# Performance work log

Measured on AMD Instinct MI355X. Metric: run time of the kernel, lower is better.

## Reference

```python
import jax, jax.numpy as jnp
import numpy as np

MAX_PAIRS = 130816  # = L*(L-1)//2 for L=512; matches init max_pairs


def setup_inputs() -> dict:
    key = jax.random.key(0)
    k1, k2, k3, k4, k5 = jax.random.split(key, 5)
    B, L, H = 32, 512, 1024
    hidden_states = jax.random.normal(k1, (B, L, H), dtype=jnp.float32)
    attention_mask = jax.random.randint(k2, (B, L), 0, 2, dtype=jnp.int32)
    special_tokens_mask = jax.random.randint(k3, (B, L), 0, 2, dtype=jnp.int32)
    # nn.Bilinear(H, H, 1): weight (1, H, H) -> squeeze to (H, H); bias (1,)
    bound = 1.0 / np.sqrt(H)
    W = jax.random.uniform(k4, (H, H), dtype=jnp.float32, minval=-bound, maxval=bound)
    b = jax.random.uniform(k5, (1,), dtype=jnp.float32, minval=-bound, maxval=bound)
    return {"hidden_states": hidden_states, "attention_mask": attention_mask,
            "special_tokens_mask": special_tokens_mask, "W": W, "b": b}


def reference(hidden_states, attention_mask, special_tokens_mask, W, b):
    # Dropout is identity in eval mode (reference assumes inference math).
    B, L, H = hidden_states.shape
    m = (attention_mask == 1) & (special_tokens_mask == 0)  # (B, L) valid AA positions

    # Bilinear score for every (t, s) pair: S[b,t,s] = h_t^T W h_s + bias
    u = jnp.einsum('blh,hk->blk', hidden_states, W)          # (B, L, H)
    S = jnp.einsum('blk,bmk->blm', u, hidden_states) + b[0]  # (B, L, L)

    # Compacted rank of each valid position (order-preserving, like nonzero()).
    r = jnp.cumsum(m.astype(jnp.int32), axis=-1) - 1          # (B, L)
    n = jnp.sum(m.astype(jnp.int32), axis=-1)[:, None, None]  # (B, 1, 1) = n_aa

    pos = jnp.arange(L, dtype=jnp.int32)
    # pair valid iff both positions are AA and t < s (compacted order preserves original order)
    valid = m[:, :, None] & m[:, None, :] & (pos[:, None] < pos[None, :])  # (B, L, L)

    i = r[:, :, None]  # compacted row index (B, L, 1)
    j = r[:, None, :]  # compacted col index (B, 1, L)
    # row-major upper-triangle (offset=1) linear index, matching torch.triu_indices order
    idx = i * (n - 1) - (i * (i - 1)) // 2 + (j - i - 1)
    idx = jnp.where(valid, idx, MAX_PAIRS)  # invalid pairs -> dump slot

    def scatter_one(s_row, ix_row):
        out = jnp.zeros((MAX_PAIRS + 1,), dtype=s_row.dtype)
        out = out.at[ix_row.reshape(-1)].set(s_row.reshape(-1))
        return out[:MAX_PAIRS]

    return jax.vmap(scatter_one)(S, idx)  # (B, MAX_PAIRS)
```

## Files before the change

kernel.cpp:

```cpp
#include <hip/hip_runtime.h>
#include <hip/hip_bf16.h>

constexpr int NB   = 32;
constexpr int LL   = 512;
constexpr int HH   = 1024;
constexpr int MAXP = 130816;
constexpr int RMAX = 256;

typedef __attribute__((ext_vector_type(8))) short short8;
typedef __attribute__((ext_vector_type(4))) float f32x4;

static __device__ inline unsigned short f2bf(float f) {
    __hip_bfloat16 h = __float2bfloat16(f);
    union { __hip_bfloat16 h; unsigned short u; } cv; cv.h = h;
    return cv.u;
}

#define GLOAD16(g, l) __builtin_amdgcn_global_load_lds( \
    (const __attribute__((address_space(1))) unsigned int*)(g), \
    (__attribute__((address_space(3))) unsigned int*)(l), 16, 0, 0)

constexpr int NGB = NB * (RMAX / 2);

__global__ __launch_bounds__(512) void prep_gather_kernel(
        const float* __restrict__ hs, const int* __restrict__ am,
        const int* __restrict__ sm, const float* __restrict__ W,
        unsigned short* __restrict__ wt, int* __restrict__ ncnt,
        unsigned short* __restrict__ hc) {
    int bi = blockIdx.x;
    if (bi < NGB) {
        int b = bi >> 7;
        int i0 = (bi & 127) * 2;
        int t = threadIdx.x;
        bool m = (am[b * LL + t] == 1) && (sm[b * LL + t] == 0);
        unsigned long long bal = __ballot(m);
        int lane = t & 63;
        int w = t >> 6;
        __shared__ int wtot[8];
        __shared__ int shg[2];
        if (lane == 0) wtot[w] = __popcll(bal);
        __syncthreads();
        int off = 0, n = 0;
        #pragma unroll
        for (int q = 0; q < 8; ++q) {
            int v = wtot[q];
            if (q < w) off += v;
            n += v;
        }
        n = min(n, RMAX);
        int npad = min(RMAX, (n + 63) & ~63);
        if (i0 == 0 && t == 0) ncnt[b] = n;
        if (i0 >= npad) return;
        int r = off + __popcll(bal & ((1ULL << lane) - 1ULL));
        if (m) {
            if (r == i0)     shg[0] = t;
            else if (r == i0 + 1) shg[1] = t;
        }
        __syncthreads();
        int half = t >> 8;
        int i = i0 + half;
        int tc = t & 255;
        ushort4 o; o.x = 0; o.y = 0; o.z = 0; o.w = 0;
        if (i < n) {
            int g = shg[half];
            float4 v = *(const float4*)(hs + ((size_t)b * LL + g) * HH + tc * 4);
            o.x = f2bf(v.x); o.y = f2bf(v.y); o.z = f2bf(v.z); o.w = f2bf(v.w);
        }
        *(ushort4*)(hc + ((size_t)b * RMAX + i) * HH + tc * 4) = o;
    } else {
        __shared__ float T[64][65];
        int tile = bi - NGB;
        int th = tile >> 4, tj = tile & 15;
        int t = threadIdx.x;
        int r = t >> 3;
        int c8 = (t & 7) * 8;
        float4 v0 = *(const float4*)(W + (size_t)(th * 64 + r) * HH + tj * 64 + c8);
        float4 v1 = *(const float4*)(W + (size_t)(th * 64 + r) * HH + tj * 64 + c8 + 4);
        T[r][c8 + 0] = v0.x; T[r][c8 + 1] = v0.y; T[r][c8 + 2] = v0.z; T[r][c8 + 3] = v0.w;
        T[r][c8 + 4] = v1.x; T[r][c8 + 5] = v1.y; T[r][c8 + 6] = v1.z; T[r][c8 + 7] = v1.w;
        __syncthreads();
        ushort4 o0, o1;
        o0.x = f2bf(T[c8 + 0][r]); o0.y = f2bf(T[c8 + 1][r]);
        o0.z = f2bf(T[c8 + 2][r]); o0.w = f2bf(T[c8 + 3][r]);
        o1.x = f2bf(T[c8 + 4][r]); o1.y = f2bf(T[c8 + 5][r]);
        o1.z = f2bf(T[c8 + 6][r]); o1.w = f2bf(T[c8 + 7][r]);
        unsigned short* dst = wt + (size_t)(tj * 64 + r) * HH + th * 64 + c8;
        *(ushort4*)dst = o0;
        *(ushort4*)(dst + 4) = o1;
    }
}

__global__ __launch_bounds__(256) void gemm1_kernel(
        const unsigned short* __restrict__ hc, const unsigned short* __restrict__ wt,
        const int* __restrict__ ncnt, unsigned short* __restrict__ uc,
        float4* __restrict__ out4, int n4) {
    constexpr int BK = 64;
    int b = blockIdx.z;
    if (b >= NB) {
        int zbid = (b - NB) * 32 + blockIdx.y * 4 + blockIdx.x;
        int gid = zbid * 256 + threadIdx.x;
        float4 z = {0.f, 0.f, 0.f, 0.f};
        for (int i = gid; i < n4; i += 65536) out4[i] = z;
        return;
    }
    int n = min(ncnt[b], RMAX);
    int it = blockIdx.x;
    if (it * 64 >= n) return;
    int kt = blockIdx.y;

    __shared__ unsigned short As[64 * BK];
    __shared__ unsigned short Bs[128 * BK];

    int tid = threadIdx.x;
    int lane = tid & 63, w = tid >> 6, wr = w >> 1, wc = w & 1;

    const unsigned short* ga = hc + ((size_t)b * RMAX + it * 64) * HH;
    const unsigned short* gb = wt + (size_t)kt * 128 * HH;

    int fa0 = tid, fa1 = tid + 256;
    int ar0 = fa0 >> 3, ar1 = fa1 >> 3;
    const unsigned short* gar0 = ga + (size_t)ar0 * HH + ((fa0 & 7) ^ (ar0 & 7)) * 8;
    const unsigned short* gar1 = ga + (size_t)ar1 * HH + ((fa1 & 7) ^ (ar1 & 7)) * 8;
    int fb0 = tid, fb1 = tid + 256, fb2 = tid + 512, fb3 = tid + 768;
    int br0 = fb0 >> 3, br1 = fb1 >> 3, br2 = fb2 >> 3, br3 = fb3 >> 3;
    const unsigned short* gbr0 = gb + (size_t)br0 * HH + ((fb0 & 7) ^ (br0 & 7)) * 8;
    const unsigned short* gbr1 = gb + (size_t)br1 * HH + ((fb1 & 7) ^ (br1 & 7)) * 8;
    const unsigned short* gbr2 = gb + (size_t)br2 * HH + ((fb2 & 7) ^ (br2 & 7)) * 8;
    const unsigned short* gbr3 = gb + (size_t)br3 * HH + ((fb3 & 7) ^ (br3 & 7)) * 8;

    f32x4 acc[2][4];
    #pragma unroll
    for (int m = 0; m < 2; ++m)
        #pragma unroll
        for (int nn = 0; nn < 4; ++nn) { acc[m][nn].x = 0.f; acc[m][nn].y = 0.f; acc[m][nn].z = 0.f; acc[m][nn].w = 0.f; }

    int fr = lane & 15;
    int khi = (lane >> 4) * 8;

    for (int k0 = 0; k0 < HH; k0 += BK) {
        GLOAD16(gar0 + k0, As + fa0 * 8);
        GLOAD16(gar1 + k0, As + fa1 * 8);
        GLOAD16(gbr0 + k0, Bs + fb0 * 8);
        GLOAD16(gbr1 + k0, Bs + fb1 * 8);
        GLOAD16(gbr2 + k0, Bs + fb2 * 8);
        GLOAD16(gbr3 + k0, Bs + fb3 * 8);
        __syncthreads();

        #pragma unroll
        for (int ks = 0; ks < 2; ++ks) {
            int k8 = ks * 32 + khi;
            short8 a0, a1, bb[4];
            {
                int row = wr * 32 + fr;
                a0 = *(const short8*)&As[row * BK + (k8 ^ ((row & 7) * 8))];
                row += 16;
                a1 = *(const short8*)&As[row * BK + (k8 ^ ((row & 7) * 8))];
            }
            #pragma unroll
            for (int nn = 0; nn < 4; ++nn) {
                int row = wc * 64 + nn * 16 + fr;
                bb[nn] = *(const short8*)&Bs[row * BK + (k8 ^ ((row & 7) * 8))];
            }
            #pragma unroll
            for (int nn = 0; nn < 4; ++nn) {
                acc[0][nn] = __builtin_amdgcn_mfma_f32_16x16x32_bf16(a0, bb[nn], acc[0][nn], 0, 0, 0);
                acc[1][nn] = __builtin_amdgcn_mfma_f32_16x16x32_bf16(a1, bb[nn], acc[1][nn], 0, 0, 0);
            }
        }
        __syncthreads();
    }

    int rowb = it * 64 + wr * 32 + (lane >> 4) * 4;
    int colb = kt * 128 + wc * 64 + (lane & 15);
    #pragma unroll
    for (int m = 0; m < 2; ++m)
        #pragma unroll
        for (int nn = 0; nn < 4; ++nn)
            #pragma unroll
            for (int r = 0; r < 4; ++r)
                uc[((size_t)b * RMAX + rowb + m * 16 + r) * HH + colb + nn * 16] = f2bf(acc[m][nn][r]);
}

__global__ __launch_bounds__(256) void gemm2_kernel(
        const unsigned short* __restrict__ uc, const unsigned short* __restrict__ hc,
        const int* __restrict__ ncnt, const float* __restrict__ bias_p,
        float* __restrict__ out) {
    constexpr int BK = 64;
    int b = blockIdx.z;
    int it = blockIdx.y, jt = blockIdx.x;
    if (jt < it) return;
    int n = min(ncnt[b], RMAX);
    if (it * 64 >= n || jt * 64 >= n) return;

    __shared__ unsigned short Us[64 * BK];
    __shared__ unsigned short Hs[64 * BK];

    int tid = threadIdx.x;
    int lane = tid & 63, w = tid >> 6, wr = w >> 1, wc = w & 1;

    const unsigned short* ga = uc + ((size_t)b * RMAX + it * 64) * HH;
    const unsigned short* gb = hc + ((size_t)b * RMAX + jt * 64) * HH;

    int f0 = tid, f1 = tid + 256;
    int r0 = f0 >> 3, r1 = f1 >> 3;
    const unsigned short* gar0 = ga + (size_t)r0 * HH + ((f0 & 7) ^ (r0 & 7)) * 8;
    const unsigned short* gar1 = ga + (size_t)r1 * HH + ((f1 & 7) ^ (r1 & 7)) * 8;
    const unsigned short* gbr0 = gb + (size_t)r0 * HH + ((f0 & 7) ^ (r0 & 7)) * 8;
    const unsigned short* gbr1 = gb + (size_t)r1 * HH + ((f1 & 7) ^ (r1 & 7)) * 8;

    f32x4 acc[2][2];
    #pragma unroll
    for (int m = 0; m < 2; ++m)
        #pragma unroll
        for (int nn = 0; nn < 2; ++nn) { acc[m][nn].x = 0.f; acc[m][nn].y = 0.f; acc[m][nn].z = 0.f; acc[m][nn].w = 0.f; }

    int fr = lane & 15;
    int khi = (lane >> 4) * 8;

    for (int k0 = 0; k0 < HH; k0 += BK) {
        GLOAD16(gar0 + k0, Us + f0 * 8);
        GLOAD16(gar1 + k0, Us + f1 * 8);
        GLOAD16(gbr0 + k0, Hs + f0 * 8);
        GLOAD16(gbr1 + k0, Hs + f1 * 8);
        __syncthreads();

        #pragma unroll
        for (int ks = 0; ks < 2; ++ks) {
            int k8 = ks * 32 + khi;
            short8 a0, a1, b0, b1;
            {
                int row = wr * 32 + fr;
                a0 = *(const short8*)&Us[row * BK + (k8 ^ ((row & 7) * 8))];
                row += 16;
                a1 = *(const short8*)&Us[row * BK + (k8 ^ ((row & 7) * 8))];
            }
            {
                int row = wc * 32 + fr;
                b0 = *(const short8*)&Hs[row * BK + (k8 ^ ((row & 7) * 8))];
                row += 16;
                b1 = *(const short8*)&Hs[row * BK + (k8 ^ ((row & 7) * 8))];
            }
            acc[0][0] = __builtin_amdgcn_mfma_f32_16x16x32_bf16(a0, b0, acc[0][0], 0, 0, 0);
            acc[0][1] = __builtin_amdgcn_mfma_f32_16x16x32_bf16(a0, b1, acc[0][1], 0, 0, 0);
            acc[1][0] = __builtin_amdgcn_mfma_f32_16x16x32_bf16(a1, b0, acc[1][0], 0, 0, 0);
            acc[1][1] = __builtin_amdgcn_mfma_f32_16x16x32_bf16(a1, b1, acc[1][1], 0, 0, 0);
        }
        __syncthreads();
    }

    float bias = bias_p[0];
    #pragma unroll
    for (int m = 0; m < 2; ++m)
        #pragma unroll
        for (int nn = 0; nn < 2; ++nn)
            #pragma unroll
            for (int r = 0; r < 4; ++r) {
                int i = it * 64 + wr * 32 + m * 16 + (lane >> 4) * 4 + r;
                int j = jt * 64 + wc * 32 + nn * 16 + (lane & 15);
                if (i < j && j < n) {
                    int idx = i * (n - 1) - (i * (i - 1)) / 2 + (j - i - 1);
                    out[(size_t)b * MAXP + idx] = acc[m][nn][r] + bias;
                }
            }
}

extern "C" void kernel_launch(void* const* d_in, const int* in_sizes, int n_in,
                              void* d_out, int out_size, void* d_ws, size_t ws_size,
                              hipStream_t stream) {
    const float* hs  = (const float*)d_in[0];
    const int*   am  = (const int*)d_in[1];
    const int*   sm  = (const int*)d_in[2];
    const float* W   = (const float*)d_in[3];
    const float* bp  = (const float*)d_in[4];
    float* out = (float*)d_out;

    char* ws = (char*)d_ws;
    int* ncnt = (int*)ws;
    unsigned short* wt = (unsigned short*)(ws + 256);
    unsigned short* hc = wt + (size_t)HH * HH;
    unsigned short* uc = hc + (size_t)NB * RMAX * HH;

    int n4 = (NB * MAXP) / 4;
    prep_gather_kernel<<<NGB + 256, 512, 0, stream>>>(hs, am, sm, W, wt, ncnt, hc);
    gemm1_kernel<<<dim3(RMAX / 64, HH / 128, NB + 8), 256, 0, stream>>>(
        hc, wt, ncnt, uc, (float4*)out, n4);
    gemm2_kernel<<<dim3(RMAX / 64, RMAX / 64, NB), 256, 0, stream>>>(uc, hc, ncnt, bp, out);
}
```

Baseline: 48.75 us.

## Fuse both GEMMs into one kernel with per-tile atomic readiness flags

Merges the u=hW GEMM and the pairwise score GEMM into one launch. Blocks that finish a u row-tile bump an agent-scope counter, and the blocks that compute scores for that row spin-wait on it before reading. The output zeroing moves into the same kernel and now clears only the tail past each batch's valid pair count instead of the whole output. This removes a kernel launch boundary and redundant zero writes, but relies on co-residency for the spin-wait to avoid deadlock and adds polling overhead.

```diff
diff --git a/kernel.cpp b/kernel.cpp
--- a/kernel.cpp
+++ b/kernel.cpp
@@ -26,7 +26,7 @@
         const float* __restrict__ hs, const int* __restrict__ am,
         const int* __restrict__ sm, const float* __restrict__ W,
         unsigned short* __restrict__ wt, int* __restrict__ ncnt,
-        unsigned short* __restrict__ hc) {
+        unsigned short* __restrict__ hc, int* __restrict__ f_uc) {
     int bi = blockIdx.x;
     if (bi < NGB) {
         int b = bi >> 7;
@@ -68,10 +68,11 @@
         }
         *(ushort4*)(hc + ((size_t)b * RMAX + i) * HH + tc * 4) = o;
     } else {
+        int t = threadIdx.x;
+        if (bi == NGB && t < NB * 4) f_uc[t] = 0;
         __shared__ float T[64][65];
         int tile = bi - NGB;
         int th = tile >> 4, tj = tile & 15;
-        int t = threadIdx.x;
         int r = t >> 3;
         int c8 = (t & 7) * 8;
         float4 v0 = *(const float4*)(W + (size_t)(th * 64 + r) * HH + tj * 64 + c8);
@@ -90,116 +91,120 @@
     }
 }
 
-__global__ __launch_bounds__(256) void gemm1_kernel(
+__global__ __launch_bounds__(256, 4) void gemm_fused_kernel(
         const unsigned short* __restrict__ hc, const unsigned short* __restrict__ wt,
         const int* __restrict__ ncnt, unsigned short* __restrict__ uc,
-        float4* __restrict__ out4, int n4) {
+        const float* __restrict__ bias_p, float* __restrict__ out,
+        int* __restrict__ f_uc) {
     constexpr int BK = 64;
+    __shared__ unsigned short As[64 * BK];
+    __shared__ unsigned short Bs[128 * BK];
+
     int b = blockIdx.z;
-    if (b >= NB) {
-        int zbid = (b - NB) * 32 + blockIdx.y * 4 + blockIdx.x;
-        int gid = zbid * 256 + threadIdx.x;
-        float4 z = {0.f, 0.f, 0.f, 0.f};
-        for (int i = gid; i < n4; i += 65536) out4[i] = z;
-        return;
-    }
     int n = min(ncnt[b], RMAX);
     int it = blockIdx.x;
-    if (it * 64 >= n) return;
     int kt = blockIdx.y;
-
-    __shared__ unsigned short As[64 * BK];
-    __shared__ unsigned short Bs[128 * BK];
-
     int tid = threadIdx.x;
     int lane = tid & 63, w = tid >> 6, wr = w >> 1, wc = w & 1;
-
-    const unsigned short* ga = hc + ((size_t)b * RMAX + it * 64) * HH;
-    const unsigned short* gb = wt + (size_t)kt * 128 * HH;
-
-    int fa0 = tid, fa1 = tid + 256;
-    int ar0 = fa0 >> 3, ar1 = fa1 >> 3;
-    const unsigned short* gar0 = ga + (size_t)ar0 * HH + ((fa0 & 7) ^ (ar0 & 7)) * 8;
-    const unsigned short* gar1 = ga + (size_t)ar1 * HH + ((fa1 & 7) ^ (ar1 & 7)) * 8;
-    int fb0 = tid, fb1 = tid + 256, fb2 = tid + 512, fb3 = tid + 768;
-    int br0 = fb0 >> 3, br1 = fb1 >> 3, br2 = fb2 >> 3, br3 = fb3 >> 3;
-    const unsigned short* gbr0 = gb + (size_t)br0 * HH + ((fb0 & 7) ^ (br0 & 7)) * 8;
-    const unsigned short* gbr1 = gb + (size_t)br1 * HH + ((fb1 & 7) ^ (br1 & 7)) * 8;
-    const unsigned short* gbr2 = gb + (size_t)br2 * HH + ((fb2 & 7) ^ (br2 & 7)) * 8;
-    const unsigned short* gbr3 = gb + (size_t)br3 * HH + ((fb3 & 7) ^ (br3 & 7)) * 8;
-
-    f32x4 acc[2][4];
-    #pragma unroll
-    for (int m = 0; m < 2; ++m)
-        #pragma unroll
-        for (int nn = 0; nn < 4; ++nn) { acc[m][nn].x = 0.f; acc[m][nn].y = 0.f; acc[m][nn].z = 0.f; acc[m][nn].w = 0.f; }
-
     int fr = lane & 15;
     int khi = (lane >> 4) * 8;
 
-    for (int k0 = 0; k0 < HH; k0 += BK) {
-        GLOAD16(gar0 + k0, As + fa0 * 8);
-        GLOAD16(gar1 + k0, As + fa1 * 8);
-        GLOAD16(gbr0 + k0, Bs + fb0 * 8);
-        GLOAD16(gbr1 + k0, Bs + fb1 * 8);
-        GLOAD16(gbr2 + k0, Bs + fb2 * 8);
-        GLOAD16(gbr3 + k0, Bs + fb3 * 8);
-        __syncthreads();
-
-        #pragma unroll
-        for (int ks = 0; ks < 2; ++ks) {
-            int k8 = ks * 32 + khi;
-            short8 a0, a1, bb[4];
-            {
-                int row = wr * 32 + fr;
-                a0 = *(const short8*)&As[row * BK + (k8 ^ ((row & 7) * 8))];
-                row += 16;
-                a1 = *(const short8*)&As[row * BK + (k8 ^ ((row & 7) * 8))];
-            }
-            #pragma unroll
-            for (int nn = 0; nn < 4; ++nn) {
-                int row = wc * 64 + nn * 16 + fr;
-                bb[nn] = *(const short8*)&Bs[row * BK + (k8 ^ ((row & 7) * 8))];
-            }
-            #pragma unroll
-            for (int nn = 0; nn < 4; ++nn) {
-                acc[0][nn] = __builtin_amdgcn_mfma_f32_16x16x32_bf16(a0, bb[nn], acc[0][nn], 0, 0, 0);
-                acc[1][nn] = __builtin_amdgcn_mfma_f32_16x16x32_bf16(a1, bb[nn], acc[1][nn], 0, 0, 0);
-            }
-        }
-        __syncthreads();
-    }
-
-    int rowb = it * 64 + wr * 32 + (lane >> 4) * 4;
-    int colb = kt * 128 + wc * 64 + (lane & 15);
-    #pragma unroll
-    for (int m = 0; m < 2; ++m)
-        #pragma unroll
-        for (int nn = 0; nn < 4; ++nn)
-            #pragma unroll
-            for (int r = 0; r < 4; ++r)
-                uc[((size_t)b * RMAX + rowb + m * 16 + r) * HH + colb + nn * 16] = f2bf(acc[m][nn][r]);
-}
-
-__global__ __launch_bounds__(256) void gemm2_kernel(
-        const unsigned short* __restrict__ uc, const unsigned short* __restrict__ hc,
-        const int* __restrict__ ncnt, const float* __restrict__ bias_p,
-        float* __restrict__ out) {
-    constexpr int BK = 64;
-    int b = blockIdx.z;
-    int it = blockIdx.y, jt = blockIdx.x;
-    if (jt < it) return;
-    int n = min(ncnt[b], RMAX);
-    if (it * 64 >= n || jt * 64 >= n) return;
-
-    __shared__ unsigned short Us[64 * BK];
-    __shared__ unsigned short Hs[64 * BK];
-
-    int tid = threadIdx.x;
-    int lane = tid & 63, w = tid >> 6, wr = w >> 1, wc = w & 1;
-
-    const unsigned short* ga = uc + ((size_t)b * RMAX + it * 64) * HH;
-    const unsigned short* gb = hc + ((size_t)b * RMAX + jt * 64) * HH;
+    if (it * 64 < n) {
+        const unsigned short* ga = hc + ((size_t)b * RMAX + it * 64) * HH;
+        const unsigned short* gb = wt + (size_t)kt * 128 * HH;
+
+        int fa0 = tid, fa1 = tid + 256;
+        int ar0 = fa0 >> 3, ar1 = fa1 >> 3;
+        const unsigned short* gar0 = ga + (size_t)ar0 * HH + ((fa0 & 7) ^ (ar0 & 7)) * 8;
+        const unsigned short* gar1 = ga + (size_t)ar1 * HH + ((fa1 & 7) ^ (ar1 & 7)) * 8;
+        int fb0 = tid, fb1 = tid + 256, fb2 = tid + 512, fb3 = tid + 768;
+        int br0 = fb0 >> 3, br1 = fb1 >> 3, br2 = fb2 >> 3, br3 = fb3 >> 3;
+        const unsigned short* gbr0 = gb + (size_t)br0 * HH + ((fb0 & 7) ^ (br0 & 7)) * 8;
+        const unsigned short* gbr1 = gb + (size_t)br1 * HH + ((fb1 & 7) ^ (br1 & 7)) * 8;
+        const unsigned short* gbr2 = gb + (size_t)br2 * HH + ((fb2 & 7) ^ (br2 & 7)) * 8;
+        const unsigned short* gbr3 = gb + (size_t)br3 * HH + ((fb3 & 7) ^ (br3 & 7)) * 8;
+
+        f32x4 acc[2][4];
+        #pragma unroll
+        for (int m = 0; m < 2; ++m)
+            #pragma unroll
+            for (int nn = 0; nn < 4; ++nn) { acc[m][nn].x = 0.f; acc[m][nn].y = 0.f; acc[m][nn].z = 0.f; acc[m][nn].w = 0.f; }
+
+        for (int k0 = 0; k0 < HH; k0 += BK) {
+            GLOAD16(gar0 + k0, As + fa0 * 8);
+            GLOAD16(gar1 + k0, As + fa1 * 8);
+            GLOAD16(gbr0 + k0, Bs + fb0 * 8);
+            GLOAD16(gbr1 + k0, Bs + fb1 * 8);
+            GLOAD16(gbr2 + k0, Bs + fb2 * 8);
+            GLOAD16(gbr3 + k0, Bs + fb3 * 8);
+            __syncthreads();
+
+            #pragma unroll
+            for (int ks = 0; ks < 2; ++ks) {
+                int k8 = ks * 32 + khi;
+                short8 a0, a1, bb[4];
+                {
+                    int row = wr * 32 + fr;
+                    a0 = *(const short8*)&As[row * BK + (k8 ^ ((row & 7) * 8))];
+                    row += 16;
+                    a1 = *(const short8*)&As[row * BK + (k8 ^ ((row & 7) * 8))];
+                }
+                #pragma unroll
+                for (int nn = 0; nn < 4; ++nn) {
+                    int row = wc * 64 + nn * 16 + fr;
+                    bb[nn] = *(const short8*)&Bs[row * BK + (k8 ^ ((row & 7) * 8))];
+                }
+                #pragma unroll
+                for (int nn = 0; nn < 4; ++nn) {
+                    acc[0][nn] = __builtin_amdgcn_mfma_f32_16x16x32_bf16(a0, bb[nn], acc[0][nn], 0, 0, 0);
+                    acc[1][nn] = __builtin_amdgcn_mfma_f32_16x16x32_bf16(a1, bb[nn], acc[1][nn], 0, 0, 0);
+                }
+            }
+            __syncthreads();
+        }
+
+        int rowb = it * 64 + wr * 32 + (lane >> 4) * 4;
+        int colb = kt * 128 + wc * 64 + (lane & 15);
+        #pragma unroll
+        for (int m = 0; m < 2; ++m)
+            #pragma unroll
+            for (int nn = 0; nn < 4; ++nn)
+                #pragma unroll
+                for (int r = 0; r < 4; ++r)
+                    uc[((size_t)b * RMAX + rowb + m * 16 + r) * HH + colb + nn * 16] = f2bf(acc[m][nn][r]);
+
+        __syncthreads();
+        if (tid == 0)
+            __hip_atomic_fetch_add(&f_uc[b * 4 + it], 1, __ATOMIC_RELEASE, __HIP_MEMORY_SCOPE_AGENT);
+    }
+
+    if (kt >= 4) {
+        int zid = (kt - 4) * 4 + it;
+        int P = n * (n - 1) / 2;
+        float* ob = out + (size_t)b * MAXP;
+        int Pa = (P + 3) & ~3;
+        if (zid == 0 && tid < (Pa - P)) ob[P + tid] = 0.f;
+        float4 z = {0.f, 0.f, 0.f, 0.f};
+        for (int qi = (Pa >> 2) + zid * 256 + tid; qi < (MAXP >> 2); qi += 16 * 256)
+            ((float4*)ob)[qi] = z;
+        return;
+    }
+
+    int it2 = kt, jt2 = it;
+    if (jt2 < it2) return;
+    if (it2 * 64 >= n || jt2 * 64 >= n) return;
+
+    if (tid == 0) {
+        while (__hip_atomic_load(&f_uc[b * 4 + it2], __ATOMIC_ACQUIRE, __HIP_MEMORY_SCOPE_AGENT) < 8)
+            __builtin_amdgcn_s_sleep(2);
+    }
+    __syncthreads();
+
+    unsigned short* Us = As;
+    unsigned short* Hs = Bs;
+
+    const unsigned short* ga = uc + ((size_t)b * RMAX + it2 * 64) * HH;
+    const unsigned short* gb = hc + ((size_t)b * RMAX + jt2 * 64) * HH;
 
     int f0 = tid, f1 = tid + 256;
     int r0 = f0 >> 3, r1 = f1 >> 3;
@@ -213,9 +218,6 @@
     for (int m = 0; m < 2; ++m)
         #pragma unroll
         for (int nn = 0; nn < 2; ++nn) { acc[m][nn].x = 0.f; acc[m][nn].y = 0.f; acc[m][nn].z = 0.f; acc[m][nn].w = 0.f; }
-
-    int fr = lane & 15;
-    int khi = (lane >> 4) * 8;
 
     for (int k0 = 0; k0 < HH; k0 += BK) {
         GLOAD16(gar0 + k0, Us + f0 * 8);
@@ -255,8 +257,8 @@
         for (int nn = 0; nn < 2; ++nn)
             #pragma unroll
             for (int r = 0; r < 4; ++r) {
-                int i = it * 64 + wr * 32 + m * 16 + (lane >> 4) * 4 + r;
-                int j = jt * 64 + wc * 32 + nn * 16 + (lane & 15);
+                int i = it2 * 64 + wr * 32 + m * 16 + (lane >> 4) * 4 + r;
+                int j = jt2 * 64 + wc * 32 + nn * 16 + (lane & 15);
                 if (i < j && j < n) {
                     int idx = i * (n - 1) - (i * (i - 1)) / 2 + (j - i - 1);
                     out[(size_t)b * MAXP + idx] = acc[m][nn][r] + bias;
@@ -276,13 +278,12 @@
 
     char* ws = (char*)d_ws;
     int* ncnt = (int*)ws;
-    unsigned short* wt = (unsigned short*)(ws + 256);
+    int* f_uc = (int*)(ws + 256);
+    unsigned short* wt = (unsigned short*)(ws + 1024);
     unsigned short* hc = wt + (size_t)HH * HH;
     unsigned short* uc = hc + (size_t)NB * RMAX * HH;
 
-    int n4 = (NB * MAXP) / 4;
-    prep_gather_kernel<<<NGB + 256, 512, 0, stream>>>(hs, am, sm, W, wt, ncnt, hc);
-    gemm1_kernel<<<dim3(RMAX / 64, HH / 128, NB + 8), 256, 0, stream>>>(
-        hc, wt, ncnt, uc, (float4*)out, n4);
-    gemm2_kernel<<<dim3(RMAX / 64, RMAX / 64, NB), 256, 0, stream>>>(uc, hc, ncnt, bp, out);
-}
+    prep_gather_kernel<<<NGB + 256, 512, 0, stream>>>(hs, am, sm, W, wt, ncnt, hc, f_uc);
+    gemm_fused_kernel<<<dim3(RMAX / 64, HH / 128, NB), 256, 0, stream>>>(
+        hc, wt, ncnt, uc, bp, out, f_uc);
+}
```

Result: slower. 95.54 us (+96.0%).
